# Optimization experiments

Measured on AMD Instinct MI355X. Metric: run time of the kernel, lower is better.

Reference implementation:

```python
import jax, jax.numpy as jnp
import numpy as np

B, T, C, H = 2, 2048, 1024, 16  # batch, seq (== block_size), n_embd, n_head
HD = C // H  # head dim


def setup_inputs() -> dict:
    key = jax.random.key(0)
    k1, k2, k3 = jax.random.split(key, 3)
    x = jax.random.normal(k1, (B, T, C), dtype=jnp.float32)
    w_attn = jax.random.normal(k2, (C, 3 * C), dtype=jnp.float32) * (1.0 / np.sqrt(C))
    b_attn = jnp.zeros((3 * C,), dtype=jnp.float32)
    w_proj = jax.random.normal(k3, (C, C), dtype=jnp.float32) * (1.0 / np.sqrt(C))
    b_proj = jnp.zeros((C,), dtype=jnp.float32)
    return {"x": x, "w_attn": w_attn, "b_attn": b_attn, "w_proj": w_proj, "b_proj": b_proj}


def reference(x, w_attn, b_attn, w_proj, b_proj):
    # qkv projection: [B,T,3C]
    qkv = x @ w_attn + b_attn
    q, k, v = jnp.split(qkv, 3, axis=-1)
    # -> [B,H,T,HD]
    def to_heads(t):
        return t.reshape(B, T, H, HD).transpose(0, 2, 1, 3)
    q, k, v = to_heads(q), to_heads(k), to_heads(v)
    scale = 1.0 / np.sqrt(HD).astype(np.float32)
    # att: [B,H,T,T]
    att = jnp.einsum("bhqd,bhkd->bhqk", q, k) * scale
    causal = jnp.tril(jnp.ones((T, T), dtype=bool))
    att = jnp.where(causal[None, None], att, -jnp.inf)
    att = jax.nn.softmax(att, axis=-1)
    # y: [B,H,T,HD] -> [B,T,C]
    y = jnp.einsum("bhqk,bhkd->bhqd", att, v)
    y = y.transpose(0, 2, 1, 3).reshape(B, T, C)
    return y @ w_proj + b_proj
```

## Files before the change

### kernel.cpp

```cpp
#include <hip/hip_runtime.h>
#include <stdint.h>

#define Bb 2
#define Tt 2048
#define Cc 1024
#define Hh 16
#define HD 64
#define C3 3072

typedef __bf16 bf16x8 __attribute__((ext_vector_type(8)));
typedef float  f32x4  __attribute__((ext_vector_type(4)));
typedef unsigned short u16;
typedef u16 u16x8 __attribute__((ext_vector_type(8)));
typedef u16 u16x4 __attribute__((ext_vector_type(4)));

#define SCALE2 0.18033688f

__device__ __forceinline__ u16 f2bf(float f) {
  union { float f; unsigned u; } v; v.f = f;
  return (u16)((v.u + 0x7fffu + ((v.u >> 16) & 1u)) >> 16);
}
__device__ __forceinline__ float bf2f(u16 a) {
  union { unsigned u; float f; } v; v.u = ((unsigned)a) << 16; return v.f;
}

__device__ __forceinline__ void gl2lds16(const void* g, void* s) {
  __builtin_amdgcn_global_load_lds(
      (__attribute__((address_space(1))) void*)(g),
      (__attribute__((address_space(3))) void*)(s), 16, 0, 0);
}

__device__ __forceinline__ bf16x8 ldb8(const u16* p) {
  return __builtin_bit_cast(bf16x8, *(const u16x8*)p);
}

template <int N>
__device__ __forceinline__ void vmwait() {
  asm volatile("s_waitcnt vmcnt(%0)" :: "n"(N) : "memory");
}
__device__ __forceinline__ void barrier_nodrain() {
  __builtin_amdgcn_s_barrier();
  __builtin_amdgcn_sched_barrier(0);
}

__global__ __launch_bounds__(256)
void prep_kernel(const float* __restrict__ x, const float* __restrict__ w_attn,
                 const float* __restrict__ w_proj, u16* __restrict__ xb,
                 u16* __restrict__ wat, u16* __restrict__ wpt) {
  __shared__ u16 tile[64][65];
  const int blk = blockIdx.x;
  const int tid = threadIdx.x;
  if (blk < 4096) {
    int i = blk * 256 + tid;
    float4 v = ((const float4*)x)[i];
    u16x4 o = { f2bf(v.x), f2bf(v.y), f2bf(v.z), f2bf(v.w) };
    ((u16x4*)xb)[i] = o;
    return;
  }
  const float* in; u16* out; int R, C, c0, r0;
  if (blk < 4096 + 768) {
    int t = blk - 4096;
    in = w_attn; out = wat; R = 1024; C = 3072;
    c0 = (t % 48) * 64; r0 = (t / 48) * 64;
  } else {
    int t = blk - 4864;
    in = w_proj; out = wpt; R = 1024; C = 1024;
    c0 = (t & 15) * 64; r0 = (t >> 4) * 64;
  }
  int xx = tid & 63, yy = tid >> 6;
  #pragma unroll
  for (int rr = yy; rr < 64; rr += 4)
    tile[rr][xx] = f2bf(in[(size_t)(r0 + rr) * C + c0 + xx]);
  __syncthreads();
  #pragma unroll
  for (int rr = yy; rr < 64; rr += 4)
    out[(size_t)(c0 + rr) * R + r0 + xx] = tile[xx][rr];
}

__global__ __launch_bounds__(512, 2)
void gemm256(const u16* __restrict__ A, const u16* __restrict__ Bt,
             const float* __restrict__ bias, u16* __restrict__ Cq,
             u16* __restrict__ Vt, int M, int N, int K) {
  __shared__ u16 As[2][256 * 64];
  __shared__ u16 Bs[2][256 * 64];
  const int tid = threadIdx.x;
  const int ln = tid & 63, w = tid >> 6;
  const int wm = w >> 2, wn = w & 3;
  const int l15 = ln & 15, lq = ln >> 4;
  const int m0 = blockIdx.y * 256, n0 = blockIdx.x * 256;

  const int lrow = ln >> 3, lchunk = ln & 7;
  const int laneoff = lrow * K + ((lchunk ^ lrow) * 8);

  f32x4 acc[8][4];
  #pragma unroll
  for (int i = 0; i < 8; ++i)
    #pragma unroll
    for (int j = 0; j < 4; ++j) acc[i][j] = (f32x4){0.f, 0.f, 0.f, 0.f};

  const int NK = K >> 6;

  auto STAGE_A = [&](int buf, int t, int mh) {
    #pragma unroll
    for (int i = 0; i < 2; ++i) {
      int r0 = i * 128 + mh * 64 + w * 8;
      gl2lds16(A + (size_t)(m0 + r0) * K + t * 64 + laneoff,
               (char*)As[buf] + (size_t)r0 * 128);
    }
  };
  auto STAGE_B = [&](int buf, int t, int nh) {
    #pragma unroll
    for (int i = 0; i < 2; ++i) {
      int r0 = (i * 2 + (w >> 2)) * 64 + nh * 32 + (w & 3) * 8;
      gl2lds16(Bt + (size_t)(n0 + r0) * K + t * 64 + laneoff,
               (char*)Bs[buf] + (size_t)r0 * 128);
    }
  };
  auto LDA = [&](const u16* base, int mh, int mfq, int kk) {
    int row = wm * 128 + mh * 64 + mfq * 16 + l15;
    return ldb8(&base[row * 64 + (((kk * 4 + lq) ^ (l15 & 7)) * 8)]);
  };
  auto LDB = [&](const u16* base, int nh, int nfq, int kk) {
    int row = wn * 64 + nh * 32 + nfq * 16 + l15;
    return ldb8(&base[row * 64 + (((kk * 4 + lq) ^ (l15 & 7)) * 8)]);
  };

  STAGE_A(0, 0, 0); STAGE_A(0, 0, 1); STAGE_B(0, 0, 0); STAGE_B(0, 0, 1);
  if (NK > 1) { STAGE_A(1, 1, 0); STAGE_A(1, 1, 1); STAGE_B(1, 1, 0); STAGE_B(1, 1, 1); }

  for (int u = 0; u < NK; ++u) {
    const int buf = u & 1;
    const u16* AsB = As[buf];
    const u16* BsB = Bs[buf];
    const bool st = (u + 2 < NK);

    if (u + 1 < NK) vmwait<8>(); else vmwait<0>();
    barrier_nodrain();
    bf16x8 afr[4][2], bfr0[2][2], bfr1[2][2];
    #pragma unroll
    for (int mfq = 0; mfq < 4; ++mfq)
      #pragma unroll
      for (int kk = 0; kk < 2; ++kk) afr[mfq][kk] = LDA(AsB, 0, mfq, kk);
    #pragma unroll
    for (int nfq = 0; nfq < 2; ++nfq)
      #pragma unroll
      for (int kk = 0; kk < 2; ++kk) bfr0[nfq][kk] = LDB(BsB, 0, nfq, kk);
    __builtin_amdgcn_s_setprio(1);
    #pragma unroll
    for (int mfq = 0; mfq < 4; ++mfq)
      #pragma unroll
      for (int nfq = 0; nfq < 2; ++nfq)
        #pragma unroll
        for (int kk = 0; kk < 2; ++kk)
          acc[mfq][nfq] = __builtin_amdgcn_mfma_f32_16x16x32_bf16(
              afr[mfq][kk], bfr0[nfq][kk], acc[mfq][nfq], 0, 0, 0);
    __builtin_amdgcn_s_setprio(0);

    barrier_nodrain();
    if (st) STAGE_A(buf, u + 2, 0);
    #pragma unroll
    for (int nfq = 0; nfq < 2; ++nfq)
      #pragma unroll
      for (int kk = 0; kk < 2; ++kk) bfr1[nfq][kk] = LDB(BsB, 1, nfq, kk);
    __builtin_amdgcn_s_setprio(1);
    #pragma unroll
    for (int mfq = 0; mfq < 4; ++mfq)
      #pragma unroll
      for (int nfq = 0; nfq < 2; ++nfq)
        #pragma unroll
        for (int kk = 0; kk < 2; ++kk)
          acc[mfq][2 + nfq] = __builtin_amdgcn_mfma_f32_16x16x32_bf16(
              afr[mfq][kk], bfr1[nfq][kk], acc[mfq][2 + nfq], 0, 0, 0);
    __builtin_amdgcn_s_setprio(0);

    barrier_nodrain();
    if (st) STAGE_B(buf, u + 2, 0);
    #pragma unroll
    for (int mfq = 0; mfq < 4; ++mfq)
      #pragma unroll
      for (int kk = 0; kk < 2; ++kk) afr[mfq][kk] = LDA(AsB, 1, mfq, kk);
    __builtin_amdgcn_s_setprio(1);
    #pragma unroll
    for (int mfq = 0; mfq < 4; ++mfq)
      #pragma unroll
      for (int nfq = 0; nfq < 2; ++nfq)
        #pragma unroll
        for (int kk = 0; kk < 2; ++kk)
          acc[4 + mfq][nfq] = __builtin_amdgcn_mfma_f32_16x16x32_bf16(
              afr[mfq][kk], bfr0[nfq][kk], acc[4 + mfq][nfq], 0, 0, 0);
    __builtin_amdgcn_s_setprio(0);

    barrier_nodrain();
    if (st) { STAGE_A(buf, u + 2, 1); STAGE_B(buf, u + 2, 1); }
    __builtin_amdgcn_s_setprio(1);
    #pragma unroll
    for (int mfq = 0; mfq < 4; ++mfq)
      #pragma unroll
      for (int nfq = 0; nfq < 2; ++nfq)
        #pragma unroll
        for (int kk = 0; kk < 2; ++kk)
          acc[4 + mfq][2 + nfq] = __builtin_amdgcn_mfma_f32_16x16x32_bf16(
              afr[mfq][kk], bfr1[nfq][kk], acc[4 + mfq][2 + nfq], 0, 0, 0);
    __builtin_amdgcn_s_setprio(0);
  }

  if (n0 >= 2048) {
    #pragma unroll
    for (int mf = 0; mf < 8; ++mf) {
      int rowb = m0 + wm * 128 + mf * 16 + lq * 4;
      int b_ = rowb >> 11, t0 = rowb & 2047;
      int tl = t0 & 63;
      int c = tl >> 4, ll = (tl >> 2) & 3;
      int pos0 = (c >> 1) * 32 + ll * 8 + (c & 1) * 4;
      size_t tdst = (size_t)(t0 & ~63) + pos0;
      #pragma unroll
      for (int nf = 0; nf < 4; ++nf) {
        int col = n0 + wn * 64 + nf * 16 + l15;
        int hd = col - 2048;
        float bsv = bias[col];
        u16x4 pk;
        #pragma unroll
        for (int r = 0; r < 4; ++r) pk[r] = f2bf(acc[mf][nf][r] + bsv);
        *(u16x4*)&Vt[(size_t)(b_ * 1024 + hd) * Tt + tdst] = pk;
      }
    }
  } else {
    #pragma unroll
    for (int mf = 0; mf < 8; ++mf) {
      int row = m0 + wm * 128 + mf * 16 + lq * 4;
      #pragma unroll
      for (int nf = 0; nf < 4; ++nf) {
        int col = n0 + wn * 64 + nf * 16 + l15;
        float bsv = bias[col];
        #pragma unroll
        for (int r = 0; r < 4; ++r)
          Cq[(size_t)(row + r) * 2048 + col] = f2bf(acc[mf][nf][r] + bsv);
      }
    }
  }
}

template <int MODE, int BN, int MINW>
__global__ __launch_bounds__(256, MINW)
void gemm_bt(const u16* __restrict__ A, const u16* __restrict__ Bt,
             const float* __restrict__ bias, void* __restrict__ Cout,
             u16* __restrict__ Vt, int M, int N, int K) {
  __shared__ u16 As[3][128 * 32];
  __shared__ u16 Bs[3][BN * 32];
  constexpr int JT = BN / 32;
  constexpr int NB = BN / 128 + 1;
  constexpr int L  = 2 + NB;
  const int tid = threadIdx.x;
  const int ln  = tid & 63;
  const int w   = tid >> 6;
  const int wm  = w >> 1, wn = w & 1;
  const int l15 = ln & 15, lq = ln >> 4;
  const int swz2 = (l15 >> 1) & 3;
  const int m0 = blockIdx.y * 128, n0 = blockIdx.x * BN;

  int aoff[2], boff[NB];
  #pragma unroll
  for (int i = 0; i < 2; ++i) {
    int s = i * 256 + tid;
    int row = s >> 2, cg = (s & 3) ^ ((s >> 3) & 3);
    aoff[i] = (m0 + row) * K + cg * 8;
  }
  #pragma unroll
  for (int i = 0; i < NB; ++i) {
    int s = i * 256 + tid;
    int row = s >> 2, cg = (s & 3) ^ ((s >> 3) & 3);
    boff[i] = (n0 + row) * K + cg * 8;
  }

  f32x4 acc[4][JT];
  #pragma unroll
  for (int i = 0; i < 4; ++i)
    #pragma unroll
    for (int j = 0; j < JT; ++j)
      acc[i][j] = (f32x4){0.f, 0.f, 0.f, 0.f};

  const int NK = K >> 5;

  auto STAGE = [&](int buf, int t) {
    const int k0 = t * 32;
    #pragma unroll
    for (int i = 0; i < 2; ++i)
      gl2lds16(A + aoff[i] + k0, (char*)As[buf] + (size_t)(i * 256 + w * 64) * 16);
    #pragma unroll
    for (int i = 0; i < NB; ++i)
      gl2lds16(Bt + boff[i] + k0, (char*)Bs[buf] + (size_t)(i * 256 + w * 64) * 16);
  };

  STAGE(0, 0);
  if (NK > 1) STAGE(1, 1);

  int cur = 0;
  for (int it = 0; it < NK; ++it) {
    if (it + 1 < NK) vmwait<L>(); else vmwait<0>();
    barrier_nodrain();
    if (it + 2 < NK) STAGE(cur == 0 ? 2 : cur - 1, it + 2);
    const u16* AsB = As[cur];
    const u16* BsB = Bs[cur];
    bf16x8 af[4], bfr[JT];
    #pragma unroll
    for (int i = 0; i < 4; ++i)
      af[i] = ldb8(&AsB[(wm * 64 + i * 16 + l15) * 32 + ((lq ^ swz2) * 8)]);
    #pragma unroll
    for (int j = 0; j < JT; ++j)
      bfr[j] = ldb8(&BsB[(wn * (BN / 2) + j * 16 + l15) * 32 + ((lq ^ swz2) * 8)]);
    #pragma unroll
    for (int i = 0; i < 4; ++i)
      #pragma unroll
      for (int j = 0; j < JT; ++j)
        acc[i][j] = __builtin_amdgcn_mfma_f32_16x16x32_bf16(af[i], bfr[j], acc[i][j], 0, 0, 0);
    cur = (cur == 2) ? 0 : cur + 1;
  }

  const int ldc = (MODE == 1) ? 2048 : N;
  #pragma unroll
  for (int i = 0; i < 4; ++i) {
    int row = m0 + wm * 64 + i * 16 + lq * 4;
    #pragma unroll
    for (int j = 0; j < JT; ++j) {
      int col = n0 + wn * (BN / 2) + j * 16 + l15;
      float bsv = bias[col];
      #pragma unroll
      for (int r = 0; r < 4; ++r) {
        float v = acc[i][j][r] + bsv;
        if (MODE == 1) ((u16*)Cout)[(size_t)(row + r) * ldc + col] = f2bf(v);
        else           ((float*)Cout)[(size_t)(row + r) * ldc + col] = v;
      }
    }
  }
}

__device__ __forceinline__ bf16x8 packp(const f32x4& a, const f32x4& b) {
  bf16x8 r;
  #pragma unroll
  for (int i = 0; i < 4; ++i) { r[i] = (__bf16)a[i]; r[i + 4] = (__bf16)b[i]; }
  return r;
}
__device__ __forceinline__ bf16x8 qscale(const u16* p) {
  u16x8 q = *(const u16x8*)p;
  u16x8 s;
  #pragma unroll
  for (int j = 0; j < 8; ++j) s[j] = f2bf(bf2f(q[j]) * SCALE2);
  return __builtin_bit_cast(bf16x8, s);
}

__global__ __launch_bounds__(256, 2)
void attn_fused(const u16* __restrict__ qk, const u16* __restrict__ vt,
                u16* __restrict__ y) {
  __shared__ u16 Ks[2][128 * 64];
  __shared__ u16 Vts[2][64 * 128];
  const int tid = threadIdx.x;
  const int ln = tid & 63, w = tid >> 6;
  const int l15 = ln & 15, lq = ln >> 4;
  const int swzK = l15 & 7;
  const int bx = blockIdx.x;
  const int bh = bx & 31;
  const int h  = bh & 15, b = bh >> 4;
  const int rr_ = bx >> 8, g = (bx >> 5) & 7;
  const int qt = (rr_ == 0) ? 31 - g : (rr_ == 1) ? 16 + g : (rr_ == 2) ? 15 - g : g;
  const int q0w = qt * 64 + w * 16;

  const u16* qbase = qk + (size_t)(b * Tt) * 2048 + h * HD;
  const u16* kbase = qk + (size_t)(b * Tt) * 2048 + 1024 + h * HD;
  const u16* vbase = vt + (size_t)(b * 1024 + h * HD) * Tt;

  int koff[4], voff[4];
  #pragma unroll
  for (int i = 0; i < 4; ++i) {
    int s = i * 256 + tid;
    koff[i] = (s >> 3) * 2048 + (((s & 7) ^ ((s >> 3) & 7)) * 8);
    voff[i] = (s >> 4) * Tt + (((s & 15) ^ ((s >> 4) & 15)) * 8);
  }

  const u16* qrA = qbase + (size_t)(q0w + l15) * 2048;
  bf16x8 qA0 = qscale(qrA + lq * 8), qA1 = qscale(qrA + 32 + lq * 8);

  bf16x8 ones;
  #pragma unroll
  for (int j = 0; j < 8; ++j) ones[j] = (__bf16)1.0f;

  f32x4 o[4];
  #pragma unroll
  for (int j = 0; j < 4; ++j) o[j] = (f32x4){0, 0, 0, 0};
  f32x4 lacc = (f32x4){0, 0, 0, 0};
  float m = -__builtin_inff();
  const int qg = q0w + l15;
  const int nkv = (qt >> 1) + 1;

  auto STAGE = [&](int buf, int t) {
    const u16* ks = kbase + (size_t)(t * 128) * 2048;
    const u16* vs = vbase + t * 128;
    #pragma unroll
    for (int i = 0; i < 4; ++i) {
      gl2lds16(ks + koff[i], (char*)Ks[buf] + (size_t)(i * 256 + w * 64) * 16);
      gl2lds16(vs + voff[i], (char*)Vts[buf] + (size_t)(i * 256 + w * 64) * 16);
    }
  };

  STAGE(0, 0);
  int cur = 0;
  for (int it = 0; it < nkv; ++it) {
    const int kk = it * 128;
    __syncthreads();
    if (it + 1 < nkv) STAGE(cur ^ 1, it + 1);
    const u16* KsB  = Ks[cur];
    const u16* VtsB = Vts[cur];

    f32x4 t[8];
    #pragma unroll
    for (int i = 0; i < 8; ++i) t[i] = (f32x4){0, 0, 0, 0};
    __builtin_amdgcn_s_setprio(1);
    #pragma unroll
    for (int i = 0; i < 8; ++i) {
      bf16x8 kf0 = ldb8(&KsB[(i * 16 + l15) * 64 + ((lq      ^ swzK) * 8)]);
      bf16x8 kf1 = ldb8(&KsB[(i * 16 + l15) * 64 + (((lq + 4) ^ swzK) * 8)]);
      t[i] = __builtin_amdgcn_mfma_f32_16x16x32_bf16(kf0, qA0, t[i], 0, 0, 0);
      t[i] = __builtin_amdgcn_mfma_f32_16x16x32_bf16(kf1, qA1, t[i], 0, 0, 0);
    }
    __builtin_amdgcn_s_setprio(0);

    if (it == nkv - 1) {
      #pragma unroll
      for (int i = 0; i < 8; ++i)
        #pragma unroll
        for (int r = 0; r < 4; ++r) {
          int kv = kk + i * 16 + lq * 4 + r;
          if (kv > qg) t[i][r] = -__builtin_inff();
        }
    }

    float a0 = fmaxf(fmaxf(t[0][0], t[0][1]), fmaxf(t[0][2], t[0][3]));
    float a1 = fmaxf(fmaxf(t[1][0], t[1][1]), fmaxf(t[1][2], t[1][3]));
    float a2 = fmaxf(fmaxf(t[2][0], t[2][1]), fmaxf(t[2][2], t[2][3]));
    float a3 = fmaxf(fmaxf(t[3][0], t[3][1]), fmaxf(t[3][2], t[3][3]));
    float a4 = fmaxf(fmaxf(t[4][0], t[4][1]), fmaxf(t[4][2], t[4][3]));
    float a5 = fmaxf(fmaxf(t[5][0], t[5][1]), fmaxf(t[5][2], t[5][3]));
    float a6 = fmaxf(fmaxf(t[6][0], t[6][1]), fmaxf(t[6][2], t[6][3]));
    float a7 = fmaxf(fmaxf(t[7][0], t[7][1]), fmaxf(t[7][2], t[7][3]));
    float mx = fmaxf(fmaxf(fmaxf(a0, a1), fmaxf(a2, a3)),
                     fmaxf(fmaxf(a4, a5), fmaxf(a6, a7)));
    mx = fmaxf(mx, __shfl_xor(mx, 16));
#if __has_builtin(__builtin_amdgcn_permlane32_swap)
    {
      unsigned mu = __builtin_bit_cast(unsigned, mx);
      auto r2 = __builtin_amdgcn_permlane32_swap(mu, mu, false, false);
      mx = fmaxf(__builtin_bit_cast(float, (unsigned)r2[0]),
                 __builtin_bit_cast(float, (unsigned)r2[1]));
    }
#else
    mx = fmaxf(mx, __shfl_xor(mx, 32));
#endif

    if (!__all(mx <= m + 8.0f)) {
      float mn = fmaxf(m, mx);
      float al = __builtin_amdgcn_exp2f(m - mn);
      m = mn;
      lacc[0] *= al;
      #pragma unroll
      for (int jd = 0; jd < 4; ++jd)
        #pragma unroll
        for (int r = 0; r < 4; ++r) o[jd][r] *= al;
    }
    #pragma unroll
    for (int i = 0; i < 8; ++i)
      #pragma unroll
      for (int r = 0; r < 4; ++r)
        t[i][r] = __builtin_amdgcn_exp2f(t[i][r] - m);

    bf16x8 pk_[4];
    #pragma unroll
    for (int ks = 0; ks < 4; ++ks) pk_[ks] = packp(t[2 * ks], t[2 * ks + 1]);

    __builtin_amdgcn_s_setprio(1);
    #pragma unroll
    for (int ks = 0; ks < 4; ++ks) {
      lacc = __builtin_amdgcn_mfma_f32_16x16x32_bf16(ones, pk_[ks], lacc, 0, 0, 0);
      #pragma unroll
      for (int jd = 0; jd < 4; ++jd) {
        int d = jd * 16 + l15;
        bf16x8 vf = ldb8(&VtsB[d * 128 + (((ks * 4 + lq) ^ l15) * 8)]);
        o[jd] = __builtin_amdgcn_mfma_f32_16x16x32_bf16(vf, pk_[ks], o[jd], 0, 0, 0);
      }
    }
    __builtin_amdgcn_s_setprio(0);
    cur ^= 1;
  }

  float inv = 1.f / lacc[0];
  const size_t ybase = (size_t)(b * Tt + q0w + l15) * Cc + h * HD;
  #pragma unroll
  for (int jd = 0; jd < 4; ++jd) {
    u16x4 pk;
    #pragma unroll
    for (int r = 0; r < 4; ++r) pk[r] = f2bf(o[jd][r] * inv);
    *(u16x4*)&y[ybase + jd * 16 + lq * 4] = pk;
  }
}

extern "C" void kernel_launch(void* const* d_in, const int* in_sizes, int n_in,
                              void* d_out, int out_size, void* d_ws, size_t ws_size,
                              hipStream_t stream) {
  const float* x      = (const float*)d_in[0];
  const float* w_attn = (const float*)d_in[1];
  const float* b_attn = (const float*)d_in[2];
  const float* w_proj = (const float*)d_in[3];
  const float* b_proj = (const float*)d_in[4];
  float* out = (float*)d_out;

  char* ws = (char*)d_ws;
  u16* xb  = (u16*)(ws + 0);
  u16* wat = (u16*)(ws + 8388608);
  u16* wpt = (u16*)(ws + 14680064);
  u16* qkb = (u16*)(ws + 16777216);
  u16* vtb = (u16*)(ws + 33554432);
  u16* yb  = (u16*)(ws + 41943040);

  prep_kernel<<<5120, 256, 0, stream>>>(x, w_attn, w_proj, xb, wat, wpt);
  gemm256<<<dim3(12, 16), 512, 0, stream>>>(xb, wat, b_attn, qkb, vtb, 4096, 3072, 1024);
  attn_fused<<<1024, 256, 0, stream>>>(qkb, vtb, yb);
  gemm_bt<0, 64, 4><<<dim3(16, 32), 256, 0, stream>>>(yb, wpt, b_proj, (void*)out, nullptr, 4096, 1024, 1024);
}
```

Baseline: 179.7 us.

## Software-pipeline QKV GEMM main loop, deferring last MFMA quadrant to next iteration

The QKV projection GEMM loop now keeps separate fragment registers for both A and B halves. The fourth MFMA quadrant of each iteration moves to the start of the next iteration, after the wait/barrier, and a tail runs it once more after the loop. This lets MFMA work overlap the buffer-ready wait and reorders LDS reads and global staging across the barriers. The cost is more live VGPRs for the duplicated fragments, and plain s_barrier replaces the nodrain variant, which may raise register pressure or change how memory waits drain.

```diff
diff --git a/kernel.cpp b/kernel.cpp
--- a/kernel.cpp
+++ b/kernel.cpp
@@ -125,6 +125,8 @@
     return ldb8(&base[row * 64 + (((kk * 4 + lq) ^ (l15 & 7)) * 8)]);
   };
 
+  bf16x8 afrA[4][2], afrB[4][2], bfrA[2][2], bfrB[2][2];
+
   STAGE_A(0, 0, 0); STAGE_A(0, 0, 1); STAGE_B(0, 0, 0); STAGE_B(0, 0, 1);
   if (NK > 1) { STAGE_A(1, 1, 0); STAGE_A(1, 1, 1); STAGE_B(1, 1, 0); STAGE_B(1, 1, 1); }
 
@@ -136,15 +138,33 @@
 
     if (u + 1 < NK) vmwait<8>(); else vmwait<0>();
     barrier_nodrain();
-    bf16x8 afr[4][2], bfr0[2][2], bfr1[2][2];
+    if (u) {
+      __builtin_amdgcn_s_setprio(1);
+      #pragma unroll
+      for (int mfq = 0; mfq < 4; ++mfq)
+        #pragma unroll
+        for (int nfq = 0; nfq < 2; ++nfq)
+          #pragma unroll
+          for (int kk = 0; kk < 2; ++kk)
+            acc[4 + mfq][2 + nfq] = __builtin_amdgcn_mfma_f32_16x16x32_bf16(
+                afrB[mfq][kk], bfrB[nfq][kk], acc[4 + mfq][2 + nfq], 0, 0, 0);
+      __builtin_amdgcn_s_setprio(0);
+    }
     #pragma unroll
     for (int mfq = 0; mfq < 4; ++mfq)
       #pragma unroll
-      for (int kk = 0; kk < 2; ++kk) afr[mfq][kk] = LDA(AsB, 0, mfq, kk);
+      for (int kk = 0; kk < 2; ++kk) afrA[mfq][kk] = LDA(AsB, 0, mfq, kk);
     #pragma unroll
     for (int nfq = 0; nfq < 2; ++nfq)
       #pragma unroll
-      for (int kk = 0; kk < 2; ++kk) bfr0[nfq][kk] = LDB(BsB, 0, nfq, kk);
+      for (int kk = 0; kk < 2; ++kk) bfrA[nfq][kk] = LDB(BsB, 0, nfq, kk);
+
+    __builtin_amdgcn_s_barrier();
+    if (st) STAGE_A(buf, u + 2, 0);
+    #pragma unroll
+    for (int nfq = 0; nfq < 2; ++nfq)
+      #pragma unroll
+      for (int kk = 0; kk < 2; ++kk) bfrB[nfq][kk] = LDB(BsB, 1, nfq, kk);
     __builtin_amdgcn_s_setprio(1);
     #pragma unroll
     for (int mfq = 0; mfq < 4; ++mfq)
@@ -153,15 +173,15 @@
         #pragma unroll
         for (int kk = 0; kk < 2; ++kk)
           acc[mfq][nfq] = __builtin_amdgcn_mfma_f32_16x16x32_bf16(
-              afr[mfq][kk], bfr0[nfq][kk], acc[mfq][nfq], 0, 0, 0);
+              afrA[mfq][kk], bfrA[nfq][kk], acc[mfq][nfq], 0, 0, 0);
     __builtin_amdgcn_s_setprio(0);
 
-    barrier_nodrain();
-    if (st) STAGE_A(buf, u + 2, 0);
-    #pragma unroll
-    for (int nfq = 0; nfq < 2; ++nfq)
-      #pragma unroll
-      for (int kk = 0; kk < 2; ++kk) bfr1[nfq][kk] = LDB(BsB, 1, nfq, kk);
+    __builtin_amdgcn_s_barrier();
+    if (st) STAGE_B(buf, u + 2, 0);
+    #pragma unroll
+    for (int mfq = 0; mfq < 4; ++mfq)
+      #pragma unroll
+      for (int kk = 0; kk < 2; ++kk) afrB[mfq][kk] = LDA(AsB, 1, mfq, kk);
     __builtin_amdgcn_s_setprio(1);
     #pragma unroll
     for (int mfq = 0; mfq < 4; ++mfq)
@@ -170,15 +190,11 @@
         #pragma unroll
         for (int kk = 0; kk < 2; ++kk)
           acc[mfq][2 + nfq] = __builtin_amdgcn_mfma_f32_16x16x32_bf16(
-              afr[mfq][kk], bfr1[nfq][kk], acc[mfq][2 + nfq], 0, 0, 0);
+              afrA[mfq][kk], bfrB[nfq][kk], acc[mfq][2 + nfq], 0, 0, 0);
     __builtin_amdgcn_s_setprio(0);
 
-    barrier_nodrain();
-    if (st) STAGE_B(buf, u + 2, 0);
-    #pragma unroll
-    for (int mfq = 0; mfq < 4; ++mfq)
-      #pragma unroll
-      for (int kk = 0; kk < 2; ++kk) afr[mfq][kk] = LDA(AsB, 1, mfq, kk);
+    __builtin_amdgcn_s_barrier();
+    if (st) { STAGE_A(buf, u + 2, 1); STAGE_B(buf, u + 2, 1); }
     __builtin_amdgcn_s_setprio(1);
     #pragma unroll
     for (int mfq = 0; mfq < 4; ++mfq)
@@ -187,22 +203,17 @@
         #pragma unroll
         for (int kk = 0; kk < 2; ++kk)
           acc[4 + mfq][nfq] = __builtin_amdgcn_mfma_f32_16x16x32_bf16(
-              afr[mfq][kk], bfr0[nfq][kk], acc[4 + mfq][nfq], 0, 0, 0);
+              afrB[mfq][kk], bfrA[nfq][kk], acc[4 + mfq][nfq], 0, 0, 0);
     __builtin_amdgcn_s_setprio(0);
-
-    barrier_nodrain();
-    if (st) { STAGE_A(buf, u + 2, 1); STAGE_B(buf, u + 2, 1); }
-    __builtin_amdgcn_s_setprio(1);
-    #pragma unroll
-    for (int mfq = 0; mfq < 4; ++mfq)
-      #pragma unroll
-      for (int nfq = 0; nfq < 2; ++nfq)
-        #pragma unroll
-        for (int kk = 0; kk < 2; ++kk)
-          acc[4 + mfq][2 + nfq] = __builtin_amdgcn_mfma_f32_16x16x32_bf16(
-              afr[mfq][kk], bfr1[nfq][kk], acc[4 + mfq][2 + nfq], 0, 0, 0);
-    __builtin_amdgcn_s_setprio(0);
-  }
+  }
+  #pragma unroll
+  for (int mfq = 0; mfq < 4; ++mfq)
+    #pragma unroll
+    for (int nfq = 0; nfq < 2; ++nfq)
+      #pragma unroll
+      for (int kk = 0; kk < 2; ++kk)
+        acc[4 + mfq][2 + nfq] = __builtin_amdgcn_mfma_f32_16x16x32_bf16(
+            afrB[mfq][kk], bfrB[nfq][kk], acc[4 + mfq][2 + nfq], 0, 0, 0);
 
   if (n0 >= 2048) {
     #pragma unroll
```

After: 178.5 us. No clear change (-0.7%).
